# Optimization experiments

Measured on AMD Instinct MI355X. Metric: run time of the kernel, lower is better.

The kernel has to match this reference:

```python
import jax, jax.numpy as jnp
import numpy as np

L, H, E, DH, T, V, B = 4, 8, 512, 64, 2048, 8000, 2
FF = 4 * E
EPS = 1e-5


def _ln(x, g, b):
    m = jnp.mean(x, -1, keepdims=True)
    v = jnp.mean((x - m) ** 2, -1, keepdims=True)
    return (x - m) * jax.lax.rsqrt(v + EPS) * g + b


def setup_inputs() -> dict:
    key = jax.random.key(0)
    ks = jax.random.split(key, 12)
    s = lambda k, shape: jax.random.normal(k, shape, jnp.float32) * 0.02
    return {
        "tokens": jax.random.randint(ks[0], (B, T), 0, V, dtype=jnp.int32),
        "tok_emb": s(ks[1], (V, E)),
        "pos_emb": s(ks[2], (T, E)),
        "Wq": s(ks[3], (L, H, E, DH)),
        "Wk": s(ks[4], (L, H, E, DH)),
        "Wv": s(ks[5], (L, H, E, DH)),
        "Wo": s(ks[6], (L, H * DH, E)),
        "bo": jnp.zeros((L, E), jnp.float32),
        "ln1_g": jnp.ones((L, E), jnp.float32),
        "ln1_b": jnp.zeros((L, E), jnp.float32),
        "ln2_g": jnp.ones((L, E), jnp.float32),
        "ln2_b": jnp.zeros((L, E), jnp.float32),
        "W1": s(ks[7], (L, E, FF)),
        "b1": jnp.zeros((L, FF), jnp.float32),
        "W2": s(ks[8], (L, FF, E)),
        "b2": jnp.zeros((L, E), jnp.float32),
        "lnf_g": jnp.ones((E,), jnp.float32),
        "lnf_b": jnp.zeros((E,), jnp.float32),
        "Wlm": s(ks[9], (E, V)),
        "blm": jnp.zeros((V,), jnp.float32),
    }


def gpt_forward(tokens, tok_emb, pos_emb, Wq, Wk, Wv, Wo, bo, ln1_g, ln1_b,
                ln2_g, ln2_b, W1, b1, W2, b2, lnf_g, lnf_b, Wlm, blm):
    b, t = tokens.shape
    x = tok_emb[tokens] + pos_emb[:t]  # [B,T,E]
    mask = jnp.tril(jnp.ones((t, t), bool))
    scale = jnp.float32(E) ** -0.5  # note: original scales by emb_size (C), not head_dim
    for l in range(L):
        h = _ln(x, ln1_g[l], ln1_b[l])
        q = jnp.einsum('bte,hed->bhtd', h, Wq[l])
        k = jnp.einsum('bte,hed->bhtd', h, Wk[l])
        v = jnp.einsum('bte,hed->bhtd', h, Wv[l])
        scores = jnp.einsum('bhtd,bhsd->bhts', q, k) * scale
        scores = jnp.where(mask, scores, -jnp.inf)
        p = jax.nn.softmax(scores, axis=-1)
        o = jnp.einsum('bhts,bhsd->bhtd', p, v)
        o = o.transpose(0, 2, 1, 3).reshape(b, t, H * DH)
        x = x + o @ Wo[l] + bo[l]
        h2 = _ln(x, ln2_g[l], ln2_b[l])
        x = x + jax.nn.relu(h2 @ W1[l] + b1[l]) @ W2[l] + b2[l]
    x = _ln(x, lnf_g, lnf_b)
    return x @ Wlm + blm  # [B,T,V]


def reference(tokens, tok_emb, pos_emb, Wq, Wk, Wv, Wo, bo, ln1_g, ln1_b,
              ln2_g, ln2_b, W1, b1, W2, b2, lnf_g, lnf_b, Wlm, blm):
    return gpt_forward(tokens, tok_emb, pos_emb, Wq, Wk, Wv, Wo, bo, ln1_g,
                       ln1_b, ln2_g, ln2_b, W1, b1, W2, b2, lnf_g, lnf_b, Wlm, blm)
```

## Files before the change

### kernel.cpp

```cpp
#include <hip/hip_runtime.h>
#include <hip/hip_bf16.h>

#define NH 8
#define EMB 512
#define HDIM 64
#define SEQ 2048
#define VOCAB 8000
#define NTOK 4096
#define FFD 2048
#define LN_EPS 1e-5f
#define SM_SCALE 0.04419417382415922f

typedef unsigned short u16;
typedef unsigned int u32;
typedef short v8s __attribute__((ext_vector_type(8)));
typedef float v4f __attribute__((ext_vector_type(4)));

typedef const __attribute__((address_space(1))) void* gas_t;
typedef __attribute__((address_space(3))) void* las_t;

struct __align__(8) U16x4 { u16 x, y, z, w; };

__device__ __forceinline__ u16 f2bf(float x) {
    union { float f; unsigned int u; } c; c.f = x;
    return (u16)((c.u + 0x7FFFu + ((c.u >> 16) & 1u)) >> 16);
}
__device__ __forceinline__ float bf2f(u16 b) {
    union { unsigned int u; float f; } c; c.u = ((unsigned int)b) << 16; return c.f;
}
__device__ __forceinline__ void splitbf(float x, u16& hi, u16& lo) {
    hi = f2bf(x);
    lo = f2bf(x - bf2f(hi));
}

__global__ __launch_bounds__(128)
void embed_kernel(const int* __restrict__ tokens, const float* __restrict__ tok_emb,
                  const float* __restrict__ pos_emb, float* __restrict__ x)
{
    const int row = blockIdx.x;
    const int t   = row & (SEQ - 1);
    const int tok = tokens[row];
    const int c   = threadIdx.x * 4;
    const float4 a = *reinterpret_cast<const float4*>(tok_emb + (size_t)tok * EMB + c);
    const float4 p = *reinterpret_cast<const float4*>(pos_emb + (size_t)t * EMB + c);
    float4 r; r.x = a.x + p.x; r.y = a.y + p.y; r.z = a.z + p.z; r.w = a.w + p.w;
    *reinterpret_cast<float4*>(x + (size_t)row * EMB + c) = r;
}

__global__ __launch_bounds__(256)
void prep_weights(const float* __restrict__ Wq, const float* __restrict__ Wk,
                  const float* __restrict__ Wv, const float* __restrict__ Wo,
                  const float* __restrict__ W1, const float* __restrict__ W2,
                  const float* __restrict__ Wlm,
                  u16* __restrict__ qkvT_h, u16* __restrict__ qkvT_l,
                  u16* __restrict__ woT_h,  u16* __restrict__ woT_l,
                  u16* __restrict__ w1T_h,  u16* __restrict__ w1T_l,
                  u16* __restrict__ w2T_h,  u16* __restrict__ w2T_l,
                  u16* __restrict__ wlmT_h, u16* __restrict__ wlmT_l)
{
    const int t = blockIdx.x;
    const float* src; u16 *dh, *dl; int R, C, ct, rt;
    if (t < 3072) {
        const int z = t >> 5, rem = t & 31;
        const int l = z / 24, r2 = z % 24, sel = r2 >> 3, h = r2 & 7;
        src = (sel == 0 ? Wq : sel == 1 ? Wk : Wv) + (size_t)(l * 8 + h) * EMB * HDIM;
        const size_t dbase = ((size_t)l * 1536 + sel * 512 + h * 64) * EMB;
        dh = qkvT_h + dbase; dl = qkvT_l + dbase;
        R = EMB; C = HDIM; ct = (rem & 1) * 32; rt = (rem >> 1) * 32;
    } else if (t < 4096) {
        const int t2 = t - 3072, z = t2 >> 8, rem = t2 & 255;
        src = Wo + (size_t)z * 262144;
        dh = woT_h + (size_t)z * 262144; dl = woT_l + (size_t)z * 262144;
        R = 512; C = 512; ct = (rem & 15) * 32; rt = (rem >> 4) * 32;
    } else if (t < 8192) {
        const int t3 = t - 4096, z = t3 >> 10, rem = t3 & 1023;
        src = W1 + (size_t)z * 1048576;
        dh = w1T_h + (size_t)z * 1048576; dl = w1T_l + (size_t)z * 1048576;
        R = 512; C = 2048; ct = (rem & 63) * 32; rt = (rem >> 6) * 32;
    } else if (t < 12288) {
        const int t4 = t - 8192, z = t4 >> 10, rem = t4 & 1023;
        src = W2 + (size_t)z * 1048576;
        dh = w2T_h + (size_t)z * 1048576; dl = w2T_l + (size_t)z * 1048576;
        R = 2048; C = 512; ct = (rem & 15) * 32; rt = (rem >> 4) * 32;
    } else {
        const int t5 = t - 12288;
        src = Wlm; dh = wlmT_h; dl = wlmT_l;
        R = 512; C = 8000; ct = (t5 % 252) * 32; rt = (t5 / 252) * 32;
    }

    __shared__ float sh[32][33];
    const int cx = threadIdx.x & 31, ry = threadIdx.x >> 5;
    #pragma unroll
    for (int i = 0; i < 4; ++i) {
        const int r = ry + i * 8;
        float v = 0.f;
        if (ct + cx < C) v = src[(size_t)(rt + r) * C + ct + cx];
        sh[r][cx] = v;
    }
    __syncthreads();
    #pragma unroll
    for (int i = 0; i < 4; ++i) {
        const int r = ry + i * 8;
        u16 hi, lo; splitbf(sh[cx][r], hi, lo);
        const size_t o = (size_t)(ct + r) * R + rt + cx;
        dh[o] = hi; dl[o] = lo;
    }
}

__global__ __launch_bounds__(256)
void ln_split_kernel(const float* __restrict__ x, const float* __restrict__ g,
                     const float* __restrict__ b, u16* __restrict__ hhi,
                     u16* __restrict__ hlo)
{
    const int row  = blockIdx.x * 4 + (threadIdx.x >> 6);
    const int lane = threadIdx.x & 63;
    const float* xp = x + (size_t)row * EMB;
    const float4 v0 = *reinterpret_cast<const float4*>(xp + lane * 4);
    const float4 v1 = *reinterpret_cast<const float4*>(xp + lane * 4 + 256);

    float s = v0.x + v0.y + v0.z + v0.w + v1.x + v1.y + v1.z + v1.w;
    #pragma unroll
    for (int off = 32; off > 0; off >>= 1) s += __shfl_xor(s, off);
    const float mean = s * (1.0f / EMB);

    float dx[8] = {v0.x - mean, v0.y - mean, v0.z - mean, v0.w - mean,
                   v1.x - mean, v1.y - mean, v1.z - mean, v1.w - mean};
    float vs = 0.f;
    #pragma unroll
    for (int u = 0; u < 8; ++u) vs = fmaf(dx[u], dx[u], vs);
    #pragma unroll
    for (int off = 32; off > 0; off >>= 1) vs += __shfl_xor(vs, off);
    const float inv = 1.0f / sqrtf(vs * (1.0f / EMB) + LN_EPS);

    const float4 g0 = *reinterpret_cast<const float4*>(g + lane * 4);
    const float4 g1 = *reinterpret_cast<const float4*>(g + lane * 4 + 256);
    const float4 b0 = *reinterpret_cast<const float4*>(b + lane * 4);
    const float4 b1 = *reinterpret_cast<const float4*>(b + lane * 4 + 256);
    float ov[8];
    ov[0] = fmaf(dx[0] * inv, g0.x, b0.x); ov[1] = fmaf(dx[1] * inv, g0.y, b0.y);
    ov[2] = fmaf(dx[2] * inv, g0.z, b0.z); ov[3] = fmaf(dx[3] * inv, g0.w, b0.w);
    ov[4] = fmaf(dx[4] * inv, g1.x, b1.x); ov[5] = fmaf(dx[5] * inv, g1.y, b1.y);
    ov[6] = fmaf(dx[6] * inv, g1.z, b1.z); ov[7] = fmaf(dx[7] * inv, g1.w, b1.w);

    U16x4 h0, l0, h1, l1;
    splitbf(ov[0], h0.x, l0.x); splitbf(ov[1], h0.y, l0.y);
    splitbf(ov[2], h0.z, l0.z); splitbf(ov[3], h0.w, l0.w);
    splitbf(ov[4], h1.x, l1.x); splitbf(ov[5], h1.y, l1.y);
    splitbf(ov[6], h1.z, l1.z); splitbf(ov[7], h1.w, l1.w);
    const size_t o = (size_t)row * EMB + lane * 4;
    *reinterpret_cast<U16x4*>(hhi + o)       = h0;
    *reinterpret_cast<U16x4*>(hhi + o + 256) = h1;
    *reinterpret_cast<U16x4*>(hlo + o)       = l0;
    *reinterpret_cast<U16x4*>(hlo + o + 256) = l1;
}

enum { EPI_QKV = 0, EPI_RES = 1, EPI_RELU_SPLIT = 2, EPI_OUT = 3 };

template<int WMC, int EPI>
__global__ __launch_bounds__(256)
void gemm_mfma(const u16* __restrict__ Ah, const u16* __restrict__ Al,
               const u16* __restrict__ Bh, const u16* __restrict__ Bl,
               const float* __restrict__ bias, int K, int N,
               float* o0,
               u16* __restrict__ u0, u16* __restrict__ u1, u16* __restrict__ u2)
{
    constexpr int BM = (WMC == 2) ? 128 : 64;
    constexpr int BN = (WMC == 0) ? 64 : 128;
    constexpr int MFRAG = (WMC == 0) ? 2 : 4;
    constexpr int NFRAG = (WMC == 2) ? 4 : 2;

    __shared__ __align__(16) u16 AhS[2][BM * 32], AlS[2][BM * 32];
    __shared__ __align__(16) u16 BhS[2][BN * 32], BlS[2][BN * 32];

    const int tid  = threadIdx.x;
    const int lane = tid & 63, w = tid >> 6;
    int moff, noff;
    if constexpr (WMC == 2)      { moff = (w >> 1) * 64; noff = (w & 1) * 64; }
    else if constexpr (WMC == 1) { moff = 0;             noff = w * 32;       }
    else                         { moff = (w >> 1) * 32; noff = (w & 1) * 32; }

    const int gy = (int)gridDim.y;
    int bid = (int)blockIdx.x * gy + (int)blockIdx.y;
    const int cpx = ((int)gridDim.x * gy) >> 3;
    bid = (bid & 7) * cpx + (bid >> 3);
    const int m0 = (bid % gy) * BM, n0 = (bid / gy) * BN;

    v4f acc[MFRAG][NFRAG];
    #pragma unroll
    for (int mi = 0; mi < MFRAG; ++mi)
        #pragma unroll
        for (int ni = 0; ni < NFRAG; ++ni) acc[mi][ni] = (v4f)0.f;

    const int arow = lane & 15, kgi = lane >> 4;

    auto stage = [&](int buf, int k0) {
        #pragma unroll
        for (int u = 0; u < BM / 64; ++u) {
            const int ch = u * 256 + tid;
            const int r = ch >> 2, cg = ch & 3;
            const int sc8 = (cg ^ ((r >> 1) & 3)) * 8;
            const size_t go = (size_t)(m0 + r) * K + k0 + sc8;
            __builtin_amdgcn_global_load_lds((gas_t)(Ah + go), (las_t)(&AhS[buf][ch * 8]), 16, 0, 0);
            __builtin_amdgcn_global_load_lds((gas_t)(Al + go), (las_t)(&AlS[buf][ch * 8]), 16, 0, 0);
        }
        #pragma unroll
        for (int u = 0; u < BN / 64; ++u) {
            const int ch = u * 256 + tid;
            const int r = ch >> 2, cg = ch & 3;
            const int sc8 = (cg ^ ((r >> 1) & 3)) * 8;
            const size_t go = (size_t)(n0 + r) * K + k0 + sc8;
            __builtin_amdgcn_global_load_lds((gas_t)(Bh + go), (las_t)(&BhS[buf][ch * 8]), 16, 0, 0);
            __builtin_amdgcn_global_load_lds((gas_t)(Bl + go), (las_t)(&BlS[buf][ch * 8]), 16, 0, 0);
        }
    };

    stage(0, 0);
    const int NK = K >> 5;
    for (int ks = 0; ks < NK; ++ks) {
        const int cur = ks & 1;
        __syncthreads();
        if (ks + 1 < NK) stage(cur ^ 1, (ks + 1) * 32);

        v8s ah[MFRAG], al[MFRAG], bh[NFRAG], bl[NFRAG];
        #pragma unroll
        for (int mi = 0; mi < MFRAG; ++mi) {
            const int ar = moff + mi * 16 + arow;
            const int idx = ar * 32 + (kgi ^ ((ar >> 1) & 3)) * 8;
            ah[mi] = *reinterpret_cast<const v8s*>(&AhS[cur][idx]);
            al[mi] = *reinterpret_cast<const v8s*>(&AlS[cur][idx]);
        }
        #pragma unroll
        for (int ni = 0; ni < NFRAG; ++ni) {
            const int br = noff + ni * 16 + arow;
            const int idx = br * 32 + (kgi ^ ((br >> 1) & 3)) * 8;
            bh[ni] = *reinterpret_cast<const v8s*>(&BhS[cur][idx]);
            bl[ni] = *reinterpret_cast<const v8s*>(&BlS[cur][idx]);
        }
        #pragma unroll
        for (int mi = 0; mi < MFRAG; ++mi)
            #pragma unroll
            for (int ni = 0; ni < NFRAG; ++ni) {
                acc[mi][ni] = __builtin_amdgcn_mfma_f32_16x16x32_bf16(ah[mi], bh[ni], acc[mi][ni], 0, 0, 0);
                acc[mi][ni] = __builtin_amdgcn_mfma_f32_16x16x32_bf16(ah[mi], bl[ni], acc[mi][ni], 0, 0, 0);
                acc[mi][ni] = __builtin_amdgcn_mfma_f32_16x16x32_bf16(al[mi], bh[ni], acc[mi][ni], 0, 0, 0);
            }
    }

    const int crow0 = (lane >> 4) * 4;
    const int ccol  = lane & 15;
    #pragma unroll
    for (int mi = 0; mi < MFRAG; ++mi) {
        const int mbase = m0 + moff + mi * 16 + crow0;
        #pragma unroll
        for (int ni = 0; ni < NFRAG; ++ni) {
            const int n = n0 + noff + ni * 16 + ccol;
            if constexpr (EPI == EPI_QKV) {
                const int sel = n >> 9, hh = (n >> 6) & 7, dd = n & 63;
                const int bbb = mbase >> 11, t = mbase & (SEQ - 1);
                if (sel == 2) {
                    U16x4 pv;
                    pv.x = f2bf(acc[mi][ni][0]); pv.y = f2bf(acc[mi][ni][1]);
                    pv.z = f2bf(acc[mi][ni][2]); pv.w = f2bf(acc[mi][ni][3]);
                    *reinterpret_cast<U16x4*>(
                        u2 + ((size_t)((bbb * NH + hh) * HDIM + dd) * SEQ + t)) = pv;
                } else {
                    u16* dst = sel ? u1 : u0;
                    const float scl = sel ? 1.0f : SM_SCALE;
                    #pragma unroll
                    for (int j = 0; j < 4; ++j) {
                        const int m = mbase + j;
                        dst[((size_t)((m >> 11) * NH + hh) * SEQ + (m & (SEQ - 1))) * HDIM + dd]
                            = f2bf(acc[mi][ni][j] * scl);
                    }
                }
            } else if constexpr (EPI == EPI_RES) {
                const float bv = bias[n];
                #pragma unroll
                for (int j = 0; j < 4; ++j) {
                    const size_t o = (size_t)(mbase + j) * N + n;
                    o0[o] = o0[o] + acc[mi][ni][j] + bv;
                }
            } else if constexpr (EPI == EPI_RELU_SPLIT) {
                const float bv = bias[n];
                #pragma unroll
                for (int j = 0; j < 4; ++j) {
                    const float v_ = fmaxf(acc[mi][ni][j] + bv, 0.f);
                    u16 hi, lo; splitbf(v_, hi, lo);
                    const size_t o = (size_t)(mbase + j) * N + n;
                    u0[o] = hi; u1[o] = lo;
                }
            } else {
                if (n < N) {
                    const float bv = bias[n];
                    #pragma unroll
                    for (int j = 0; j < 4; ++j)
                        o0[(size_t)(mbase + j) * N + n] = acc[mi][ni][j] + bv;
                }
            }
        }
    }
}

__global__ __launch_bounds__(128)
void attn_mfma(const u16* __restrict__ qg, const u16* __restrict__ kg,
               const u16* __restrict__ vg, u16* __restrict__ ohi,
               u16* __restrict__ olo)
{
    __shared__ __align__(16) u16 KT[2][4096];
    __shared__ __align__(16) u16 VT[2][4096];
    __shared__ __align__(16) u16 PL[2][2048];

    const int tid = threadIdx.x, lane = tid & 63, w = tid >> 6;
    const int g = lane >> 4, c = lane & 15;
    const int bh = blockIdx.y;
    const int qt = (bh & 8) ? (int)blockIdx.x : 31 - (int)blockIdx.x;
    const int bb = bh >> 3, hh = bh & 7;

    const u16* qb = qg + (size_t)bh * (SEQ * HDIM);
    const u16* kb = kg + (size_t)bh * (SEQ * HDIM);
    const u16* vb = vg + (size_t)bh * (HDIM * SEQ);

    int soffK[4], soffV[4];
    #pragma unroll
    for (int i = 0; i < 4; ++i) {
        const int ch = w * 256 + i * 64 + lane;
        const int r = ch >> 3;
        const int sc_ = ((ch & 7) ^ (r & 7)) * 8;
        soffK[i] = r * HDIM + sc_;
        soffV[i] = r * SEQ + sc_;
    }

    v8s qreg[2][2];
    const int q0 = qt * 64 + w * 32;
    #pragma unroll
    for (int nf = 0; nf < 2; ++nf)
        #pragma unroll
        for (int ch = 0; ch < 2; ++ch)
            qreg[nf][ch] = *reinterpret_cast<const v8s*>(
                qb + (size_t)(q0 + nf * 16 + c) * HDIM + ch * 32 + g * 8);

    v4f oacc[4][2];
    #pragma unroll
    for (int mf = 0; mf < 4; ++mf)
        #pragma unroll
        for (int nf = 0; nf < 2; ++nf) oacc[mf][nf] = (v4f)0.f;
    float m_[2] = {-3.0e38f, -3.0e38f}, l_[2] = {0.f, 0.f};

    #pragma unroll
    for (int i = 0; i < 4; ++i) {
        const int ch = w * 256 + i * 64 + lane;
        __builtin_amdgcn_global_load_lds((gas_t)(kb + soffK[i]), (las_t)(&KT[0][ch * 8]), 16, 0, 0);
        __builtin_amdgcn_global_load_lds((gas_t)(vb + soffV[i]), (las_t)(&VT[0][ch * 8]), 16, 0, 0);
    }
    __syncthreads();

    for (int kt = 0; kt <= qt; ++kt) {
        const int cur = kt & 1;
        if (kt < qt) {
            const int kn = kt + 1;
            #pragma unroll
            for (int i = 0; i < 4; ++i) {
                const int ch = w * 256 + i * 64 + lane;
                __builtin_amdgcn_global_load_lds((gas_t)(kb + (size_t)kn * 64 * HDIM + soffK[i]),
                                                 (las_t)(&KT[cur ^ 1][ch * 8]), 16, 0, 0);
                __builtin_amdgcn_global_load_lds((gas_t)(vb + (size_t)kn * 64 + soffV[i]),
                                                 (las_t)(&VT[cur ^ 1][ch * 8]), 16, 0, 0);
            }
        }

        v4f sacc[4][2];
        #pragma unroll
        for (int mf = 0; mf < 4; ++mf)
            #pragma unroll
            for (int nf = 0; nf < 2; ++nf) sacc[mf][nf] = (v4f)0.f;
        #pragma unroll
        for (int ch = 0; ch < 2; ++ch) {
            v8s kf[4];
            #pragma unroll
            for (int mf = 0; mf < 4; ++mf) {
                const int row = mf * 16 + c;
                int idx = row * 64 + ch * 32 + g * 8;
                idx ^= (row & 7) << 3;
                kf[mf] = *reinterpret_cast<const v8s*>(&KT[cur][idx]);
            }
            #pragma unroll
            for (int mf = 0; mf < 4; ++mf)
                #pragma unroll
                for (int nf = 0; nf < 2; ++nf)
                    sacc[mf][nf] = __builtin_amdgcn_mfma_f32_16x16x32_bf16(
                        kf[mf], qreg[nf][ch], sacc[mf][nf], 0, 0, 0);
        }

        if (kt == qt) {
            #pragma unroll
            for (int mf = 0; mf < 4; ++mf)
                #pragma unroll
                for (int nf = 0; nf < 2; ++nf)
                    #pragma unroll
                    for (int j = 0; j < 4; ++j) {
                        const int kvl = mf * 16 + g * 4 + j;
                        const int ql  = w * 32 + nf * 16 + c;
                        if (kvl > ql) sacc[mf][nf][j] = -3.0e38f;
                    }
        }

        #pragma unroll
        for (int nf = 0; nf < 2; ++nf) {
            float pmax = -3.0e38f;
            #pragma unroll
            for (int mf = 0; mf < 4; ++mf)
                #pragma unroll
                for (int j = 0; j < 4; ++j) pmax = fmaxf(pmax, sacc[mf][nf][j]);
            pmax = fmaxf(pmax, __shfl_xor(pmax, 16));
            pmax = fmaxf(pmax, __shfl_xor(pmax, 32));
            const float mnew = fmaxf(m_[nf], pmax);
            const float sc = __expf(m_[nf] - mnew);
            m_[nf] = mnew;
            float rs = 0.f;
            #pragma unroll
            for (int mf = 0; mf < 4; ++mf) {
                float p0 = __expf(sacc[mf][nf][0] - mnew);
                float p1 = __expf(sacc[mf][nf][1] - mnew);
                float p2 = __expf(sacc[mf][nf][2] - mnew);
                float p3 = __expf(sacc[mf][nf][3] - mnew);
                rs += (p0 + p1) + (p2 + p3);
                const u32 w0 = (u32)f2bf(p0) | ((u32)f2bf(p1) << 16);
                const u32 w1 = (u32)f2bf(p2) | ((u32)f2bf(p3) << 16);
                const int qrow = nf * 16 + c;
                int idx0 = qrow * 64 + mf * 16 + g * 4;
                idx0 ^= (qrow & 7) << 3;
                *reinterpret_cast<u32*>(&PL[w][idx0]) = w0;
                int idx1 = qrow * 64 + mf * 16 + g * 4 + 2;
                idx1 ^= (qrow & 7) << 3;
                *reinterpret_cast<u32*>(&PL[w][idx1]) = w1;
            }
            rs += __shfl_xor(rs, 16);
            rs += __shfl_xor(rs, 32);
            l_[nf] = l_[nf] * sc + rs;
            #pragma unroll
            for (int mf = 0; mf < 4; ++mf)
                #pragma unroll
                for (int j = 0; j < 4; ++j) oacc[mf][nf][j] *= sc;
        }

        #pragma unroll
        for (int ch = 0; ch < 2; ++ch) {
            v8s vf[4], pf[2];
            #pragma unroll
            for (int mf = 0; mf < 4; ++mf) {
                const int row = mf * 16 + c;
                int idx = row * 64 + ch * 32 + g * 8;
                idx ^= (row & 7) << 3;
                vf[mf] = *reinterpret_cast<const v8s*>(&VT[cur][idx]);
            }
            #pragma unroll
            for (int nf = 0; nf < 2; ++nf) {
                const int qrow = nf * 16 + c;
                int idx = qrow * 64 + ch * 32 + g * 8;
                idx ^= (qrow & 7) << 3;
                pf[nf] = *reinterpret_cast<const v8s*>(&PL[w][idx]);
            }
            #pragma unroll
            for (int mf = 0; mf < 4; ++mf)
                #pragma unroll
                for (int nf = 0; nf < 2; ++nf)
                    oacc[mf][nf] = __builtin_amdgcn_mfma_f32_16x16x32_bf16(
                        vf[mf], pf[nf], oacc[mf][nf], 0, 0, 0);
        }
        __syncthreads();
    }

    #pragma unroll
    for (int nf = 0; nf < 2; ++nf) {
        const float inv = 1.0f / l_[nf];
        const size_t row = (size_t)bb * SEQ + q0 + nf * 16 + c;
        #pragma unroll
        for (int mf = 0; mf < 4; ++mf) {
            float v0 = oacc[mf][nf][0] * inv, v1 = oacc[mf][nf][1] * inv;
            float v2 = oacc[mf][nf][2] * inv, v3 = oacc[mf][nf][3] * inv;
            U16x4 hv, lv;
            splitbf(v0, hv.x, lv.x); splitbf(v1, hv.y, lv.y);
            splitbf(v2, hv.z, lv.z); splitbf(v3, hv.w, lv.w);
            const size_t off = row * EMB + hh * HDIM + mf * 16 + g * 4;
            *reinterpret_cast<U16x4*>(ohi + off) = hv;
            *reinterpret_cast<U16x4*>(olo + off) = lv;
        }
    }
}

extern "C" void kernel_launch(void* const* d_in, const int* in_sizes, int n_in,
                              void* d_out, int out_size, void* d_ws, size_t ws_size,
                              hipStream_t stream)
{
    const int*   tokens  = (const int*)  d_in[0];
    const float* tok_emb = (const float*)d_in[1];
    const float* pos_emb = (const float*)d_in[2];
    const float* Wq      = (const float*)d_in[3];
    const float* Wk      = (const float*)d_in[4];
    const float* Wv      = (const float*)d_in[5];
    const float* Wo      = (const float*)d_in[6];
    const float* bo      = (const float*)d_in[7];
    const float* ln1_g   = (const float*)d_in[8];
    const float* ln1_b   = (const float*)d_in[9];
    const float* ln2_g   = (const float*)d_in[10];
    const float* ln2_b   = (const float*)d_in[11];
    const float* W1      = (const float*)d_in[12];
    const float* b1      = (const float*)d_in[13];
    const float* W2      = (const float*)d_in[14];
    const float* b2      = (const float*)d_in[15];
    const float* lnf_g   = (const float*)d_in[16];
    const float* lnf_b   = (const float*)d_in[17];
    const float* Wlm     = (const float*)d_in[18];
    const float* blm     = (const float*)d_in[19];
    float* out = (float*)d_out;

    const size_t NE = (size_t)NTOK * EMB;
    const size_t NF = (size_t)NTOK * FFD;
    float* x   = (float*)d_ws;
    float* zr  = x + NE;
    u16* qb16  = (u16*)zr;
    u16* kb16  = qb16 + NE;
    u16* vb16  = kb16 + NE;
    u16* ohi   = vb16 + NE;
    u16* olo   = ohi + NE;
    u16* ffhi  = (u16*)zr;
    u16* fflo  = ffhi + NF;
    u16* hhi   = (u16*)(zr + 4 * NE);
    u16* hlo   = hhi + NE;

    const size_t SQKV = (size_t)4 * 1536 * 512;
    const size_t SWO  = (size_t)4 * 512 * 512;
    const size_t SW1  = (size_t)4 * 2048 * 512;
    const size_t SLM  = (size_t)8064 * 512;
    u16* qkvT_h = hlo + NE;        u16* qkvT_l = qkvT_h + SQKV;
    u16* woT_h  = qkvT_l + SQKV;   u16* woT_l  = woT_h + SWO;
    u16* w1T_h  = woT_l + SWO;     u16* w1T_l  = w1T_h + SW1;
    u16* w2T_h  = w1T_l + SW1;     u16* w2T_l  = w2T_h + SW1;
    u16* wlmT_h = w2T_l + SW1;     u16* wlmT_l = wlmT_h + SLM;

    prep_weights<<<16320, 256, 0, stream>>>(Wq, Wk, Wv, Wo, W1, W2, Wlm,
                                            qkvT_h, qkvT_l, woT_h, woT_l,
                                            w1T_h, w1T_l, w2T_h, w2T_l,
                                            wlmT_h, wlmT_l);

    embed_kernel<<<NTOK, 128, 0, stream>>>(tokens, tok_emb, pos_emb, x);

    for (int l = 0; l < 4; ++l) {
        ln_split_kernel<<<NTOK / 4, 256, 0, stream>>>(x, ln1_g + l * EMB, ln1_b + l * EMB,
                                                      hhi, hlo);
        gemm_mfma<2, EPI_QKV><<<dim3(12, 32), 256, 0, stream>>>(
            hhi, hlo, qkvT_h + (size_t)l * 1536 * 512, qkvT_l + (size_t)l * 1536 * 512,
            nullptr, EMB, 1536, nullptr, qb16, kb16, vb16);

        attn_mfma<<<dim3(32, 16), 128, 0, stream>>>(qb16, kb16, vb16, ohi, olo);

        gemm_mfma<0, EPI_RES><<<dim3(8, 64), 256, 0, stream>>>(
            ohi, olo, woT_h + (size_t)l * 262144, woT_l + (size_t)l * 262144,
            bo + l * EMB, EMB, EMB, x, nullptr, nullptr, nullptr);

        ln_split_kernel<<<NTOK / 4, 256, 0, stream>>>(x, ln2_g + l * EMB, ln2_b + l * EMB,
                                                      hhi, hlo);
        gemm_mfma<2, EPI_RELU_SPLIT><<<dim3(16, 32), 256, 0, stream>>>(
            hhi, hlo, w1T_h + (size_t)l * 1048576, w1T_l + (size_t)l * 1048576,
            b1 + l * FFD, EMB, FFD, nullptr, ffhi, fflo, nullptr);

        gemm_mfma<0, EPI_RES><<<dim3(8, 64), 256, 0, stream>>>(
            ffhi, fflo, w2T_h + (size_t)l * 1048576, w2T_l + (size_t)l * 1048576,
            b2 + l * EMB, FFD, EMB, x, nullptr, nullptr, nullptr);
    }

    ln_split_kernel<<<NTOK / 4, 256, 0, stream>>>(x, lnf_g, lnf_b, hhi, hlo);

    gemm_mfma<2, EPI_OUT><<<dim3(63, 32), 256, 0, stream>>>(
        hhi, hlo, wlmT_h, wlmT_l, blm, EMB, VOCAB, out, nullptr, nullptr, nullptr);
}
```

Before: 1.085 ms.

## Halve attention query tile to 32 rows and double grid; raise MFMA priority

Each attention block now handles 32 query rows (16 per wave) instead of 64, doubling the grid to 64x16. The goal is better occupancy and load balance across CUs. The cost is that K/V tiles are reloaded twice as often overall, and the causal mask for the last tile depends on which half the query tile falls in. s_setprio raises wave priority around the MFMA sections, and the QKV GEMM switches to a smaller tile variant with twice the row blocks.

```diff
diff --git a/kernel.cpp b/kernel.cpp
--- a/kernel.cpp
+++ b/kernel.cpp
@@ -308,13 +308,14 @@
 {
     __shared__ __align__(16) u16 KT[2][4096];
     __shared__ __align__(16) u16 VT[2][4096];
-    __shared__ __align__(16) u16 PL[2][2048];
+    __shared__ __align__(16) u16 PL[2][1024];
 
     const int tid = threadIdx.x, lane = tid & 63, w = tid >> 6;
     const int g = lane >> 4, c = lane & 15;
     const int bh = blockIdx.y;
-    const int qt = (bh & 8) ? (int)blockIdx.x : 31 - (int)blockIdx.x;
+    const int qt = (bh & 8) ? (int)blockIdx.x : 63 - (int)blockIdx.x;
     const int bb = bh >> 3, hh = bh & 7;
+    const int nkv = (qt >> 1) + 1;
 
     const u16* qb = qg + (size_t)bh * (SEQ * HDIM);
     const u16* kb = kg + (size_t)bh * (SEQ * HDIM);
@@ -330,21 +331,17 @@
         soffV[i] = r * SEQ + sc_;
     }
 
-    v8s qreg[2][2];
-    const int q0 = qt * 64 + w * 32;
-    #pragma unroll
-    for (int nf = 0; nf < 2; ++nf)
-        #pragma unroll
-        for (int ch = 0; ch < 2; ++ch)
-            qreg[nf][ch] = *reinterpret_cast<const v8s*>(
-                qb + (size_t)(q0 + nf * 16 + c) * HDIM + ch * 32 + g * 8);
-
-    v4f oacc[4][2];
-    #pragma unroll
-    for (int mf = 0; mf < 4; ++mf)
-        #pragma unroll
-        for (int nf = 0; nf < 2; ++nf) oacc[mf][nf] = (v4f)0.f;
-    float m_[2] = {-3.0e38f, -3.0e38f}, l_[2] = {0.f, 0.f};
+    v8s qreg[2];
+    const int qrow = qt * 32 + w * 16 + c;
+    #pragma unroll
+    for (int ch = 0; ch < 2; ++ch)
+        qreg[ch] = *reinterpret_cast<const v8s*>(
+            qb + (size_t)qrow * HDIM + ch * 32 + g * 8);
+
+    v4f oacc[4];
+    #pragma unroll
+    for (int mf = 0; mf < 4; ++mf) oacc[mf] = (v4f)0.f;
+    float m_ = -3.0e38f, l_ = 0.f;
 
     #pragma unroll
     for (int i = 0; i < 4; ++i) {
@@ -354,9 +351,9 @@
     }
     __syncthreads();
 
-    for (int kt = 0; kt <= qt; ++kt) {
+    for (int kt = 0; kt < nkv; ++kt) {
         const int cur = kt & 1;
-        if (kt < qt) {
+        if (kt + 1 < nkv) {
             const int kn = kt + 1;
             #pragma unroll
             for (int i = 0; i < 4; ++i) {
@@ -368,11 +365,10 @@
             }
         }
 
-        v4f sacc[4][2];
-        #pragma unroll
-        for (int mf = 0; mf < 4; ++mf)
-            #pragma unroll
-            for (int nf = 0; nf < 2; ++nf) sacc[mf][nf] = (v4f)0.f;
+        v4f sacc[4];
+        #pragma unroll
+        for (int mf = 0; mf < 4; ++mf) sacc[mf] = (v4f)0.f;
+        __builtin_amdgcn_s_setprio(1);
         #pragma unroll
         for (int ch = 0; ch < 2; ++ch) {
             v8s kf[4];
@@ -385,67 +381,63 @@
             }
             #pragma unroll
             for (int mf = 0; mf < 4; ++mf)
-                #pragma unroll
-                for (int nf = 0; nf < 2; ++nf)
-                    sacc[mf][nf] = __builtin_amdgcn_mfma_f32_16x16x32_bf16(
-                        kf[mf], qreg[nf][ch], sacc[mf][nf], 0, 0, 0);
-        }
-
-        if (kt == qt) {
+                sacc[mf] = __builtin_amdgcn_mfma_f32_16x16x32_bf16(
+                    kf[mf], qreg[ch], sacc[mf], 0, 0, 0);
+        }
+        __builtin_amdgcn_s_setprio(0);
+
+        if (kt == nkv - 1) {
+            const int qloc = ((qt & 1) << 5) + w * 16 + c;
             #pragma unroll
             for (int mf = 0; mf < 4; ++mf)
                 #pragma unroll
-                for (int nf = 0; nf < 2; ++nf)
-                    #pragma unroll
-                    for (int j = 0; j < 4; ++j) {
-                        const int kvl = mf * 16 + g * 4 + j;
-                        const int ql  = w * 32 + nf * 16 + c;
-                        if (kvl > ql) sacc[mf][nf][j] = -3.0e38f;
-                    }
-        }
-
-        #pragma unroll
-        for (int nf = 0; nf < 2; ++nf) {
+                for (int j = 0; j < 4; ++j) {
+                    const int kvl = mf * 16 + g * 4 + j;
+                    if (kvl > qloc) sacc[mf][j] = -3.0e38f;
+                }
+        }
+
+        {
             float pmax = -3.0e38f;
             #pragma unroll
             for (int mf = 0; mf < 4; ++mf)
                 #pragma unroll
-                for (int j = 0; j < 4; ++j) pmax = fmaxf(pmax, sacc[mf][nf][j]);
+                for (int j = 0; j < 4; ++j) pmax = fmaxf(pmax, sacc[mf][j]);
             pmax = fmaxf(pmax, __shfl_xor(pmax, 16));
             pmax = fmaxf(pmax, __shfl_xor(pmax, 32));
-            const float mnew = fmaxf(m_[nf], pmax);
-            const float sc = __expf(m_[nf] - mnew);
-            m_[nf] = mnew;
+            const float mnew = fmaxf(m_, pmax);
+            const float sc = __expf(m_ - mnew);
+            m_ = mnew;
             float rs = 0.f;
             #pragma unroll
             for (int mf = 0; mf < 4; ++mf) {
-                float p0 = __expf(sacc[mf][nf][0] - mnew);
-                float p1 = __expf(sacc[mf][nf][1] - mnew);
-                float p2 = __expf(sacc[mf][nf][2] - mnew);
-                float p3 = __expf(sacc[mf][nf][3] - mnew);
+                float p0 = __expf(sacc[mf][0] - mnew);
+                float p1 = __expf(sacc[mf][1] - mnew);
+                float p2 = __expf(sacc[mf][2] - mnew);
+                float p3 = __expf(sacc[mf][3] - mnew);
                 rs += (p0 + p1) + (p2 + p3);
                 const u32 w0 = (u32)f2bf(p0) | ((u32)f2bf(p1) << 16);
                 const u32 w1 = (u32)f2bf(p2) | ((u32)f2bf(p3) << 16);
-                const int qrow = nf * 16 + c;
-                int idx0 = qrow * 64 + mf * 16 + g * 4;
-                idx0 ^= (qrow & 7) << 3;
+                int idx0 = c * 64 + mf * 16 + g * 4;
+                idx0 ^= (c & 7) << 3;
                 *reinterpret_cast<u32*>(&PL[w][idx0]) = w0;
-                int idx1 = qrow * 64 + mf * 16 + g * 4 + 2;
-                idx1 ^= (qrow & 7) << 3;
+                int idx1 = c * 64 + mf * 16 + g * 4 + 2;
+                idx1 ^= (c & 7) << 3;
                 *reinterpret_cast<u32*>(&PL[w][idx1]) = w1;
             }
             rs += __shfl_xor(rs, 16);
             rs += __shfl_xor(rs, 32);
-            l_[nf] = l_[nf] * sc + rs;
+            l_ = l_ * sc + rs;
             #pragma unroll
             for (int mf = 0; mf < 4; ++mf)
                 #pragma unroll
-                for (int j = 0; j < 4; ++j) oacc[mf][nf][j] *= sc;
-        }
-
+                for (int j = 0; j < 4; ++j) oacc[mf][j] *= sc;
+        }
+
+        __builtin_amdgcn_s_setprio(1);
         #pragma unroll
         for (int ch = 0; ch < 2; ++ch) {
-            v8s vf[4], pf[2];
+            v8s vf[4], pf;
             #pragma unroll
             for (int mf = 0; mf < 4; ++mf) {
                 const int row = mf * 16 + c;
@@ -453,31 +445,27 @@
                 idx ^= (row & 7) << 3;
                 vf[mf] = *reinterpret_cast<const v8s*>(&VT[cur][idx]);
             }
-            #pragma unroll
-            for (int nf = 0; nf < 2; ++nf) {
-                const int qrow = nf * 16 + c;
-                int idx = qrow * 64 + ch * 32 + g * 8;
-                idx ^= (qrow & 7) << 3;
-                pf[nf] = *reinterpret_cast<const v8s*>(&PL[w][idx]);
+            {
+                int idx = c * 64 + ch * 32 + g * 8;
+                idx ^= (c & 7) << 3;
+                pf = *reinterpret_cast<const v8s*>(&PL[w][idx]);
             }
             #pragma unroll
             for (int mf = 0; mf < 4; ++mf)
-                #pragma unroll
-                for (int nf = 0; nf < 2; ++nf)
-                    oacc[mf][nf] = __builtin_amdgcn_mfma_f32_16x16x32_bf16(
-                        vf[mf], pf[nf], oacc[mf][nf], 0, 0, 0);
-        }
+                oacc[mf] = __builtin_amdgcn_mfma_f32_16x16x32_bf16(
+                    vf[mf], pf, oacc[mf], 0, 0, 0);
+        }
+        __builtin_amdgcn_s_setprio(0);
         __syncthreads();
     }
 
-    #pragma unroll
-    for (int nf = 0; nf < 2; ++nf) {
-        const float inv = 1.0f / l_[nf];
-        const size_t row = (size_t)bb * SEQ + q0 + nf * 16 + c;
+    {
+        const float inv = 1.0f / l_;
+        const size_t row = (size_t)bb * SEQ + qrow;
         #pragma unroll
         for (int mf = 0; mf < 4; ++mf) {
-            float v0 = oacc[mf][nf][0] * inv, v1 = oacc[mf][nf][1] * inv;
-            float v2 = oacc[mf][nf][2] * inv, v3 = oacc[mf][nf][3] * inv;
+            float v0 = oacc[mf][0] * inv, v1 = oacc[mf][1] * inv;
+            float v2 = oacc[mf][2] * inv, v3 = oacc[mf][3] * inv;
             U16x4 hv, lv;
             splitbf(v0, hv.x, lv.x); splitbf(v1, hv.y, lv.y);
             splitbf(v2, hv.z, lv.z); splitbf(v3, hv.w, lv.w);
@@ -548,11 +536,11 @@
     for (int l = 0; l < 4; ++l) {
         ln_split_kernel<<<NTOK / 4, 256, 0, stream>>>(x, ln1_g + l * EMB, ln1_b + l * EMB,
                                                       hhi, hlo);
-        gemm_mfma<2, EPI_QKV><<<dim3(12, 32), 256, 0, stream>>>(
+        gemm_mfma<1, EPI_QKV><<<dim3(12, 64), 256, 0, stream>>>(
             hhi, hlo, qkvT_h + (size_t)l * 1536 * 512, qkvT_l + (size_t)l * 1536 * 512,
             nullptr, EMB, 1536, nullptr, qb16, kb16, vb16);
 
-        attn_mfma<<<dim3(32, 16), 128, 0, stream>>>(qb16, kb16, vb16, ohi, olo);
+        attn_mfma<<<dim3(64, 16), 128, 0, stream>>>(qb16, kb16, vb16, ohi, olo);
 
         gemm_mfma<0, EPI_RES><<<dim3(8, 64), 256, 0, stream>>>(
             ohi, olo, woT_h + (size_t)l * 262144, woT_l + (size_t)l * 262144,
```

After: 1.032 ms. -4.9%, faster.
